# Kernel optimization log

Measured on AMD Instinct MI355X. Metric: run time of the kernel, lower is better.

Reference implementation:

```python
import jax, jax.numpy as jnp
import numpy as np

EMB_DIM = 1024
NUM_HEAD = 16
HEAD_DIM = EMB_DIM // NUM_HEAD
B, S = 2, 2048


def setup_inputs() -> dict:
    key = jax.random.key(0)
    ks = jax.random.split(key, 10)
    scale = 1.0 / np.sqrt(EMB_DIM)
    x = jax.random.normal(ks[0], (B, S, EMB_DIM), dtype=jnp.float32)
    # causal mask: 1 = keep, 0 = masked out (torch masked_fill(mask == 0, -inf))
    mask = jnp.tril(jnp.ones((S, S), dtype=jnp.int32))[None, None, :, :]
    def lin(kw, kb):
        W = jax.random.uniform(kw, (EMB_DIM, EMB_DIM), jnp.float32, -scale, scale)
        b = jax.random.uniform(kb, (EMB_DIM,), jnp.float32, -scale, scale)
        return W, b
    Wq, bq = lin(ks[1], ks[2])
    Wk, bk = lin(ks[3], ks[4])
    Wv, bv = lin(ks[5], ks[6])
    Wo, bo = lin(ks[7], ks[8])
    return {"x": x, "mask": mask, "Wq": Wq, "bq": bq, "Wk": Wk, "bk": bk,
            "Wv": Wv, "bv": bv, "Wo": Wo, "bo": bo}


def reference(x, mask, Wq, bq, Wk, bk, Wv, bv, Wo, bo):
    Bsz, Sq, _ = x.shape
    # projections; torch Linear: y = x @ W^T + b
    def proj(W, b):
        y = jnp.einsum('bse,fe->bsf', x, W) + b
        return y.reshape(Bsz, Sq, NUM_HEAD, HEAD_DIM).transpose(0, 2, 1, 3)  # [B,H,S,D]
    q = proj(Wq, bq)
    k = proj(Wk, bk)
    v = proj(Wv, bv)
    scaling = jnp.asarray(HEAD_DIM ** 0.5, x.dtype)
    scores = jnp.einsum('bhqd,bhkd->bhqk', q, k) / scaling  # [B,H,S,S]
    scores = jnp.where(mask == 0, -jnp.inf, scores)
    attn = jax.nn.softmax(scores, axis=-1)
    out = jnp.einsum('bhqk,bhkd->bhqd', attn, v)
    out = out.transpose(0, 2, 1, 3).reshape(Bsz, Sq, EMB_DIM)
    return jnp.einsum('bse,fe->bsf', out, Wo) + bo
```

## Files before the change

### kernel.cpp

```cpp
#include <hip/hip_runtime.h>

typedef unsigned short u16;
typedef __attribute__((ext_vector_type(8))) __bf16 bf16x8;
typedef __attribute__((ext_vector_type(8))) short  short8;
typedef __attribute__((ext_vector_type(4))) short  short4v;
typedef __attribute__((ext_vector_type(4))) float  floatx4;
typedef __attribute__((ext_vector_type(4))) int    intx4;
typedef __attribute__((ext_vector_type(2))) int    intx2;

constexpr int Bc = 2, Sc = 2048, Ec = 1024, Hc = 16, Dc = 64;
constexpr int Mc = Bc * Sc;

#define QSCALE  0.18033688011112042f

__device__ __forceinline__ u16 f2b(float f) {
  union { float f; unsigned u; } c; c.f = f;
  unsigned u = c.u;
  return (u16)((u + 0x7fffu + ((u >> 16) & 1u)) >> 16);
}
__device__ __forceinline__ short8 ld8(const u16* p) { return *(const short8*)p; }

__device__ __forceinline__ int cvt_pk(float lo, float hi) {
  int r;
  asm("v_cvt_pk_bf16_f32 %0, %1, %2" : "=v"(r) : "v"(lo), "v"(hi));
  return r;
}

__device__ __forceinline__ floatx4 mfma16(short8 a, short8 b, floatx4 c) {
  return __builtin_amdgcn_mfma_f32_16x16x32_bf16(
      __builtin_bit_cast(bf16x8, a), __builtin_bit_cast(bf16x8, b), c, 0, 0, 0);
}

__device__ __forceinline__ void async16(const u16* g, u16* l) {
  __builtin_amdgcn_global_load_lds(
      (const __attribute__((address_space(1))) void*)g,
      (__attribute__((address_space(3))) void*)l, 16, 0, 0);
}

__global__ __launch_bounds__(256) void cvt_kernel(
    const float* __restrict__ x,  const float* __restrict__ Wq,
    const float* __restrict__ Wk, const float* __restrict__ Wv,
    const float* __restrict__ Wo, u16* __restrict__ dst) {
  const size_t i = ((size_t)blockIdx.x * 256 + threadIdx.x) * 4;
  const int seg = (int)(i >> 20);
  const float* src;
  size_t off;
  if (seg < 4)       { src = x;  off = i; }
  else if (seg == 4) { src = Wq; off = i - ((size_t)4 << 20); }
  else if (seg == 5) { src = Wk; off = i - ((size_t)5 << 20); }
  else if (seg == 6) { src = Wv; off = i - ((size_t)6 << 20); }
  else               { src = Wo; off = i - ((size_t)7 << 20); }
  floatx4 v = *(const floatx4*)(src + off);
  intx2 o;
  o[0] = cvt_pk(v[0], v[1]);
  o[1] = cvt_pk(v[2], v[3]);
  *(intx2*)(dst + i) = o;
}

__device__ __forceinline__ void gemm128d(
    const u16* __restrict__ A, const u16* __restrict__ B, int K,
    int m0, int n0, u16* As, u16* Bs, floatx4 acc[4][4]) {
  const int t = threadIdx.x;
  const int w = t >> 6, lane = t & 63;
  const int wm = w & 1, wn = w >> 1;
  const int quad = lane >> 4, l16 = lane & 15;
  const int r = t >> 2;
  const int c = ((t & 3) ^ ((t >> 3) & 3)) * 8;
  const int rs = (quad ^ ((l16 >> 1) & 3)) * 8;

  const u16* ap0 = A + (size_t)(m0 + r) * K + c;
  const u16* ap1 = A + (size_t)(m0 + 64 + r) * K + c;
  const u16* bp0 = B + (size_t)(n0 + r) * K + c;
  const u16* bp1 = B + (size_t)(n0 + 64 + r) * K + c;
  u16* const al0 = As + w * 512;
  u16* const al1 = As + 2048 + w * 512;
  u16* const bl0 = Bs + w * 512;
  u16* const bl1 = Bs + 2048 + w * 512;

#pragma unroll
  for (int i = 0; i < 4; ++i)
#pragma unroll
    for (int j = 0; j < 4; ++j) acc[i][j] = 0.f;

  async16(ap0, al0);
  async16(ap1, al1);
  async16(bp0, bl0);
  async16(bp1, bl1);

  int cur = 0;
  for (int k0 = 0; k0 < K; k0 += 32) {
    if (k0 + 32 < K) {
      const int nb = cur ^ 1;
      async16(ap0 + k0 + 32, al0 + nb * 4096);
      async16(ap1 + k0 + 32, al1 + nb * 4096);
      async16(bp0 + k0 + 32, bl0 + nb * 4096);
      async16(bp1 + k0 + 32, bl1 + nb * 4096);
      __builtin_amdgcn_sched_barrier(0);
      asm volatile("s_waitcnt vmcnt(4)");
    } else {
      asm volatile("s_waitcnt vmcnt(0)");
    }
    __builtin_amdgcn_s_barrier();
    __builtin_amdgcn_sched_barrier(0);

    short8 af[4], bfr[4];
#pragma unroll
    for (int i = 0; i < 4; ++i)
      af[i]  = *(const short8*)(As + cur * 4096 +
                                (wm * 64 + i * 16 + l16) * 32 + rs);
#pragma unroll
    for (int j = 0; j < 4; ++j)
      bfr[j] = *(const short8*)(Bs + cur * 4096 +
                                (wn * 64 + j * 16 + l16) * 32 + rs);
#pragma unroll
    for (int i = 0; i < 4; ++i)
#pragma unroll
      for (int j = 0; j < 4; ++j)
        acc[i][j] = mfma16(af[i], bfr[j], acc[i][j]);

    __builtin_amdgcn_sched_barrier(0);
    __builtin_amdgcn_s_barrier();
    cur ^= 1;
  }
}

__device__ __forceinline__ void gemm64x128(
    const u16* __restrict__ A, const u16* __restrict__ B, int K,
    int m0, int n0, u16* As, u16* Bs, floatx4 acc[2][4]) {
  const int t = threadIdx.x;
  const int w = t >> 6, lane = t & 63;
  const int wm = w & 1, wn = w >> 1;
  const int quad = lane >> 4, l16 = lane & 15;
  const int r = t >> 2;
  const int c = ((t & 3) ^ ((t >> 3) & 3)) * 8;
  const int rs = (quad ^ ((l16 >> 1) & 3)) * 8;

  const u16* ap  = A + (size_t)(m0 + r) * K + c;
  const u16* bp0 = B + (size_t)(n0 + r) * K + c;
  const u16* bp1 = B + (size_t)(n0 + 64 + r) * K + c;
  u16* const al  = As + w * 512;
  u16* const bl0 = Bs + w * 512;
  u16* const bl1 = Bs + 2048 + w * 512;

#pragma unroll
  for (int i = 0; i < 2; ++i)
#pragma unroll
    for (int j = 0; j < 4; ++j) acc[i][j] = 0.f;

  async16(ap,  al);
  async16(bp0, bl0);
  async16(bp1, bl1);

  int cur = 0;
  for (int k0 = 0; k0 < K; k0 += 32) {
    if (k0 + 32 < K) {
      const int nb = cur ^ 1;
      async16(ap  + k0 + 32, al  + nb * 2048);
      async16(bp0 + k0 + 32, bl0 + nb * 4096);
      async16(bp1 + k0 + 32, bl1 + nb * 4096);
      __builtin_amdgcn_sched_barrier(0);
      asm volatile("s_waitcnt vmcnt(3)");
    } else {
      asm volatile("s_waitcnt vmcnt(0)");
    }
    __builtin_amdgcn_s_barrier();
    __builtin_amdgcn_sched_barrier(0);

    short8 af[2], bfr[4];
#pragma unroll
    for (int i = 0; i < 2; ++i)
      af[i]  = *(const short8*)(As + cur * 2048 +
                                (wm * 32 + i * 16 + l16) * 32 + rs);
#pragma unroll
    for (int j = 0; j < 4; ++j)
      bfr[j] = *(const short8*)(Bs + cur * 4096 +
                                (wn * 64 + j * 16 + l16) * 32 + rs);
#pragma unroll
    for (int i = 0; i < 2; ++i)
#pragma unroll
      for (int j = 0; j < 4; ++j)
        acc[i][j] = mfma16(af[i], bfr[j], acc[i][j]);

    __builtin_amdgcn_sched_barrier(0);
    __builtin_amdgcn_s_barrier();
    cur ^= 1;
  }
}

__global__ __launch_bounds__(256, 4) void qkv_mm(
    const u16* __restrict__ xb, const u16* __restrict__ Wb,
    const float* __restrict__ bq, const float* __restrict__ bk,
    const float* __restrict__ bv,
    u16* __restrict__ Q, u16* __restrict__ K_, u16* __restrict__ Vt) {
  __shared__ __align__(16) u16 As[8192], Bs[8192];
  const int z = blockIdx.z;
  const u16* W = Wb + ((size_t)z << 20);
  const float* bias = (z == 0) ? bq : (z == 1) ? bk : bv;
  const int m0 = blockIdx.y * 128, n0 = blockIdx.x * 128;

  floatx4 acc[4][4];
  gemm128d(xb, W, Ec, m0, n0, As, Bs, acc);

  const int t = threadIdx.x, w = t >> 6, lane = t & 63;
  const int wm = w & 1, wn = w >> 1, quad = lane >> 4, l16 = lane & 15;
#pragma unroll
  for (int i = 0; i < 4; ++i)
#pragma unroll
    for (int j = 0; j < 4; ++j)
#pragma unroll
      for (int rr = 0; rr < 4; ++rr) {
        const int row = m0 + wm * 64 + i * 16 + quad * 4 + rr;
        const int col = n0 + wn * 64 + j * 16 + l16;
        float v = acc[i][j][rr] + bias[col];
        if (z == 0) v *= QSCALE;
        const int bb = row >> 11, s = row & (Sc - 1);
        const int h = col >> 6, d = col & (Dc - 1), bh = bb * Hc + h;
        if (z < 2) ((z == 0) ? Q : K_)[((size_t)bh * Sc + s) * Dc + d] = f2b(v);
        else {
          const int sp = (s & ~31) | ((s & 12) << 1) | ((s & 16) >> 2) | (s & 3);
          Vt[((size_t)bh * Dc + d) * Sc + sp] = f2b(v);
        }
      }
}

__global__ __launch_bounds__(256, 6) void proj_mm(
    const u16* __restrict__ O, const u16* __restrict__ Wob,
    const float* __restrict__ bias, float* __restrict__ out) {
  __shared__ __align__(16) u16 As[4096], Bs[8192];
  const int m0 = blockIdx.y * 64, n0 = blockIdx.x * 128;

  floatx4 acc[2][4];
  gemm64x128(O, Wob, Ec, m0, n0, As, Bs, acc);

  const int t = threadIdx.x, w = t >> 6, lane = t & 63;
  const int wm = w & 1, wn = w >> 1, quad = lane >> 4, l16 = lane & 15;
#pragma unroll
  for (int i = 0; i < 2; ++i)
#pragma unroll
    for (int j = 0; j < 4; ++j)
#pragma unroll
      for (int rr = 0; rr < 4; ++rr) {
        const int row = m0 + wm * 32 + i * 16 + quad * 4 + rr;
        const int col = n0 + wn * 64 + j * 16 + l16;
        out[(size_t)row * Ec + col] = acc[i][j][rr] + bias[col];
      }
}

__global__ __launch_bounds__(256, 4) void attn_kernel(
    const u16* __restrict__ Q, const u16* __restrict__ K,
    const u16* __restrict__ Vt, u16* __restrict__ O) {
  const int v  = blockIdx.x & 31, g8 = blockIdx.x >> 5, kk = blockIdx.y;
  const int q1 = (kk & 2) ? ((v + 8) & 31) : v;
  const int qt = (kk & 1) ? (31 - q1) : q1;
  const int q0 = qt * 64;
  const int bh = kk * 8 + g8;
  const int bb = bh >> 4, h = bh & 15;

  const u16* Qh = Q  + (size_t)bh * Sc * Dc;
  const u16* Kh = K  + (size_t)bh * Sc * Dc;
  const u16* Vh = Vt + (size_t)bh * Dc * Sc;

  const int t = threadIdx.x;
  const int w = t >> 6, lane = t & 63;
  const int quad = lane >> 4, l16 = lane & 15;

  __shared__ __align__(16) u16 Ks[8192];
  __shared__ __align__(16) u16 Vs[8192];

  const int sr = w * 8 + (lane >> 3);
  const int sb = (lane & 7) ^ (lane >> 3);
  const int swz = l16 & 7;

  const u16* qrow_p = Qh + (size_t)(q0 + w * 16 + l16) * Dc;
  const short8 aq0 = ld8(qrow_p + quad * 8);
  const short8 aq1 = ld8(qrow_p + 32 + quad * 8);

  float   lrow = 0.f;
  floatx4 oacc[4];
#pragma unroll
  for (int dt = 0; dt < 4; ++dt) oacc[dt] = 0.f;

  for (int kt = 0; kt <= q0; kt += 128) {
#pragma unroll
    for (int st = 0; st < 2; ++st)
#pragma unroll
      for (int it = 0; it < 2; ++it) {
        const int r = it * 32 + sr;
        async16(Kh + (size_t)(kt + st * 64 + r) * Dc + sb * 8,
                Ks + st * 4096 + it * 2048 + w * 512);
        async16(Vh + (size_t)r * Sc + kt + st * 64 + sb * 8,
                Vs + st * 4096 + it * 2048 + w * 512);
      }
    __syncthreads();

    floatx4 sacc[8];
#pragma unroll
    for (int g = 0; g < 8; ++g) sacc[g] = 0.f;
#pragma unroll
    for (int ks = 0; ks < 2; ++ks) {
      const short8 bq = ks ? aq1 : aq0;
#pragma unroll
      for (int g = 0; g < 8; ++g) {
        const short8 a = *(const short8*)(
            Ks + (g >> 2) * 4096 + ((g & 3) * 16 + l16) * 64 +
            (((ks * 4 + quad) ^ swz) * 8));
        sacc[g] = mfma16(a, bq, sacc[g]);
      }
    }

    const bool diag = (kt + 128 > q0);
    const int thr = q0 + w * 16 + l16 - kt - 4 * quad;
#pragma unroll
    for (int g = 0; g < 8; ++g)
#pragma unroll
      for (int r = 0; r < 4; ++r) {
        float pv = exp2f(sacc[g][r]);
        if (diag && (16 * g + r > thr)) pv = 0.f;
        lrow += pv;
        sacc[g][r] = pv;
      }

    short8 pa[4];
#pragma unroll
    for (int c = 0; c < 4; ++c) {
      intx4 wd;
      wd[0] = cvt_pk(sacc[2 * c][0],     sacc[2 * c][1]);
      wd[1] = cvt_pk(sacc[2 * c][2],     sacc[2 * c][3]);
      wd[2] = cvt_pk(sacc[2 * c + 1][0], sacc[2 * c + 1][1]);
      wd[3] = cvt_pk(sacc[2 * c + 1][2], sacc[2 * c + 1][3]);
      pa[c] = __builtin_bit_cast(short8, wd);
    }

#pragma unroll
    for (int c = 0; c < 4; ++c) {
      const int st = c >> 1, kcl = c & 1;
#pragma unroll
      for (int dt = 0; dt < 4; ++dt) {
        const short8 b = *(const short8*)(
            Vs + st * 4096 + (dt * 16 + l16) * 64 +
            (((kcl * 4 + quad) ^ swz) * 8));
        oacc[dt] = mfma16(pa[c], b, oacc[dt]);
      }
    }
    __syncthreads();
  }

  lrow += __shfl_xor(lrow, 16);
  lrow += __shfl_xor(lrow, 32);
  float rs[4];
#pragma unroll
  for (int r = 0; r < 4; ++r)
    rs[r] = 1.f / __shfl(lrow, quad * 4 + r, 16);

#pragma unroll
  for (int dt = 0; dt < 4; ++dt) {
#pragma unroll
    for (int r = 0; r < 4; ++r) {
      const int qrow = q0 + w * 16 + quad * 4 + r;
      O[((size_t)(bb * Sc + qrow)) * Ec + h * Dc + dt * 16 + l16] =
          f2b(oacc[dt][r] * rs[r]);
    }
  }
}

extern "C" void kernel_launch(void* const* d_in, const int* in_sizes, int n_in,
                              void* d_out, int out_size, void* d_ws, size_t ws_size,
                              hipStream_t stream) {
  const float* x  = (const float*)d_in[0];
  const float* Wq = (const float*)d_in[2];
  const float* bq = (const float*)d_in[3];
  const float* Wk = (const float*)d_in[4];
  const float* bk = (const float*)d_in[5];
  const float* Wv = (const float*)d_in[6];
  const float* bv = (const float*)d_in[7];
  const float* Wo = (const float*)d_in[8];
  const float* bo = (const float*)d_in[9];

  const size_t MiE = (size_t)Mc * Ec;
  u16* Q  = (u16*)d_ws;
  u16* K  = Q  + MiE;
  u16* Vt = K  + MiE;
  u16* O  = Vt + MiE;
  u16* xb = O  + MiE;
  u16* Wb = xb + MiE;
  u16* Wob = Wb + ((size_t)3 << 20);

  cvt_kernel<<<8192, 256, 0, stream>>>(x, Wq, Wk, Wv, Wo, xb);
  qkv_mm<<<dim3(Ec / 128, Mc / 128, 3), 256, 0, stream>>>(
      xb, Wb, bq, bk, bv, Q, K, Vt);
  attn_kernel<<<dim3(256, 4), 256, 0, stream>>>(Q, K, Vt, O);
  proj_mm<<<dim3(Ec / 128, Mc / 64), 256, 0, stream>>>(O, Wob, bo, (float*)d_out);
}
```

Measured before the change: 199.1 us.

## Double-buffer attention K/V tiles with 64-key steps and async prefetch

Splits the attention key loop from 128-key steps into 64-key steps. It uses the two LDS halves as a ping-pong double buffer, so the async load of the next K/V tile overlaps the MFMA and softmax work on the current tile. Manual vmcnt waits and raw s_barrier replace __syncthreads, and s_setprio raises wave priority around the MFMA blocks. Launch bounds go from 4 to 5 blocks per CU, which adds register pressure and the risk of spills. The extra barriers per key step may also cost more than the overlap gains.

```diff
diff --git a/kernel.cpp b/kernel.cpp
--- a/kernel.cpp
+++ b/kernel.cpp
@@ -246,7 +246,7 @@
       }
 }
 
-__global__ __launch_bounds__(256, 4) void attn_kernel(
+__global__ __launch_bounds__(256, 5) void attn_kernel(
     const u16* __restrict__ Q, const u16* __restrict__ K,
     const u16* __restrict__ Vt, u16* __restrict__ O) {
   const int v  = blockIdx.x & 31, g8 = blockIdx.x >> 5, kk = blockIdx.y;
@@ -280,38 +280,52 @@
 #pragma unroll
   for (int dt = 0; dt < 4; ++dt) oacc[dt] = 0.f;
 
-  for (int kt = 0; kt <= q0; kt += 128) {
-#pragma unroll
-    for (int st = 0; st < 2; ++st)
-#pragma unroll
-      for (int it = 0; it < 2; ++it) {
-        const int r = it * 32 + sr;
-        async16(Kh + (size_t)(kt + st * 64 + r) * Dc + sb * 8,
-                Ks + st * 4096 + it * 2048 + w * 512);
-        async16(Vh + (size_t)r * Sc + kt + st * 64 + sb * 8,
-                Vs + st * 4096 + it * 2048 + w * 512);
-      }
-    __syncthreads();
-
-    floatx4 sacc[8];
-#pragma unroll
-    for (int g = 0; g < 8; ++g) sacc[g] = 0.f;
+#define ATTN_STAGE(kt_, buf_)                                                  \
+  {                                                                            \
+    _Pragma("unroll")                                                          \
+    for (int it = 0; it < 2; ++it) {                                           \
+      const int r_ = it * 32 + sr;                                             \
+      async16(Kh + (size_t)((kt_) + r_) * Dc + sb * 8,                         \
+              Ks + (buf_)*4096 + it * 2048 + w * 512);                         \
+      async16(Vh + (size_t)r_ * Sc + (kt_) + sb * 8,                           \
+              Vs + (buf_)*4096 + it * 2048 + w * 512);                         \
+    }                                                                          \
+  }
+
+  ATTN_STAGE(0, 0);
+  int cur = 0;
+  for (int kt = 0; kt <= q0; kt += 64) {
+    if (kt < q0) {
+      ATTN_STAGE(kt + 64, cur ^ 1);
+      __builtin_amdgcn_sched_barrier(0);
+      asm volatile("s_waitcnt vmcnt(4)");
+    } else {
+      asm volatile("s_waitcnt vmcnt(0)");
+    }
+    __builtin_amdgcn_s_barrier();
+    __builtin_amdgcn_sched_barrier(0);
+
+    floatx4 sacc[4];
+#pragma unroll
+    for (int g = 0; g < 4; ++g) sacc[g] = 0.f;
+    __builtin_amdgcn_s_setprio(1);
 #pragma unroll
     for (int ks = 0; ks < 2; ++ks) {
       const short8 bq = ks ? aq1 : aq0;
 #pragma unroll
-      for (int g = 0; g < 8; ++g) {
+      for (int g = 0; g < 4; ++g) {
         const short8 a = *(const short8*)(
-            Ks + (g >> 2) * 4096 + ((g & 3) * 16 + l16) * 64 +
+            Ks + cur * 4096 + (g * 16 + l16) * 64 +
             (((ks * 4 + quad) ^ swz) * 8));
         sacc[g] = mfma16(a, bq, sacc[g]);
       }
     }
-
-    const bool diag = (kt + 128 > q0);
+    __builtin_amdgcn_s_setprio(0);
+
+    const bool diag = (kt == q0);
     const int thr = q0 + w * 16 + l16 - kt - 4 * quad;
 #pragma unroll
-    for (int g = 0; g < 8; ++g)
+    for (int g = 0; g < 4; ++g)
 #pragma unroll
       for (int r = 0; r < 4; ++r) {
         float pv = exp2f(sacc[g][r]);
@@ -320,9 +334,9 @@
         sacc[g][r] = pv;
       }
 
-    short8 pa[4];
-#pragma unroll
-    for (int c = 0; c < 4; ++c) {
+    short8 pa[2];
+#pragma unroll
+    for (int c = 0; c < 2; ++c) {
       intx4 wd;
       wd[0] = cvt_pk(sacc[2 * c][0],     sacc[2 * c][1]);
       wd[1] = cvt_pk(sacc[2 * c][2],     sacc[2 * c][3]);
@@ -331,18 +345,22 @@
       pa[c] = __builtin_bit_cast(short8, wd);
     }
 
-#pragma unroll
-    for (int c = 0; c < 4; ++c) {
-      const int st = c >> 1, kcl = c & 1;
+    __builtin_amdgcn_s_setprio(1);
+#pragma unroll
+    for (int c = 0; c < 2; ++c) {
 #pragma unroll
       for (int dt = 0; dt < 4; ++dt) {
         const short8 b = *(const short8*)(
-            Vs + st * 4096 + (dt * 16 + l16) * 64 +
-            (((kcl * 4 + quad) ^ swz) * 8));
+            Vs + cur * 4096 + (dt * 16 + l16) * 64 +
+            (((c * 4 + quad) ^ swz) * 8));
         oacc[dt] = mfma16(pa[c], b, oacc[dt]);
       }
     }
-    __syncthreads();
+    __builtin_amdgcn_s_setprio(0);
+
+    __builtin_amdgcn_sched_barrier(0);
+    __builtin_amdgcn_s_barrier();
+    cur ^= 1;
   }
 
   lrow += __shfl_xor(lrow, 16);
```

Result: slower. 207.2 us (+4.1%).
